# Optimization experiments

Measured on AMD Instinct MI355X. Metric: run time of the kernel, lower is better.

The kernel has to match this reference:

```python
import jax, jax.numpy as jnp
import numpy as np

N_NEURONS = 256
P_MAX = 8
N_BLOCKS = P_MAX + 1
HIDDEN = 32
BATCH = 8192


def setup_inputs() -> dict:
    key = jax.random.key(0)
    ks = jax.random.split(key, 9)
    z = jax.random.normal(ks[0], (BATCH, N_BLOCKS * N_NEURONS), dtype=jnp.float32)
    # Per-block ScalarMLP params, stacked over the n_blocks axis.
    s1 = 1.0 / np.sqrt(N_NEURONS)
    s2 = 1.0 / np.sqrt(HIDDEN)
    gW1 = jax.random.uniform(ks[1], (N_BLOCKS, N_NEURONS, HIDDEN), jnp.float32, -s1, s1)
    gb1 = jax.random.uniform(ks[2], (N_BLOCKS, HIDDEN), jnp.float32, -s1, s1)
    gW2 = jax.random.uniform(ks[3], (N_BLOCKS, HIDDEN, HIDDEN), jnp.float32, -s2, s2)
    gb2 = jax.random.uniform(ks[4], (N_BLOCKS, HIDDEN), jnp.float32, -s2, s2)
    gW3 = jax.random.uniform(ks[5], (N_BLOCKS, HIDDEN), jnp.float32, -s2, s2)
    gb3 = jax.random.uniform(ks[6], (N_BLOCKS,), jnp.float32, -s2, s2)
    # Lag coupling matrices W_r ~ U(-init_scale, init_scale), init_scale=0.1
    W = jax.random.uniform(ks[7], (P_MAX, N_NEURONS, N_NEURONS), jnp.float32, -0.1, 0.1)
    return {"z": z, "gW1": gW1, "gb1": gb1, "gW2": gW2, "gb2": gb2,
            "gW3": gW3, "gb3": gb3, "W": W}


def _energy(z, gW1, gb1, gW2, gb2, gW3, gb3, W):
    B = z.shape[0]
    blocks = z.reshape(B, N_BLOCKS, N_NEURONS)           # (B, K, n)
    # Per-block ScalarMLP energies (all blocks at once).
    h1 = jax.nn.silu(jnp.einsum('bkn,knh->bkh', blocks, gW1) + gb1)   # (B, K, H)
    h2 = jax.nn.silu(jnp.einsum('bkh,khg->bkg', h1, gW2) + gb2)       # (B, K, H)
    e = jnp.einsum('bkh,kh->bk', h2, gW3) + gb3                        # (B, K)
    # Bilinear lag couplings: z_future^T W_r z_{lag-r}, r = 1..p_max.
    z_future = blocks[:, P_MAX, :]                                     # (B, n)
    lags = blocks[:, :P_MAX, :][:, ::-1, :]                            # (B, p, n), index r-1 == block p_max-r
    cross = jnp.einsum('bi,rij,brj->b', z_future, W, lags)             # (B,)
    return e.sum(axis=-1) + cross                                      # (B,)


def reference(z, gW1, gb1, gW2, gb2, gW3, gb3, W):
    # Score s(z) = -grad_z U(z); sum over batch gives per-sample grads
    # since energies are independent across samples.
    grad_z = jax.grad(lambda zz: _energy(zz, gW1, gb1, gW2, gb2, gW3, gb3, W).sum())(z)
    return -grad_z
```

## Files before the change

### kernel.cpp

```cpp
#include <hip/hip_runtime.h>
#include <hip/hip_bf16.h>
#include <math.h>

#define BATCH 8192
#define NB 9
#define NN 256
#define PMAX 8
#define HID 32
#define ZDIM 2304

typedef short bf16x8 __attribute__((ext_vector_type(8)));
typedef float f32x4 __attribute__((ext_vector_type(4)));

static __device__ inline unsigned short f2bf(float f) {
    __hip_bfloat16 h = __float2bfloat16(f);
    return *reinterpret_cast<unsigned short*>(&h);
}

static __device__ inline uint4 pack8(float4 a, float4 b) {
    uint4 u;
    u.x = (unsigned)f2bf(a.x) | ((unsigned)f2bf(a.y) << 16);
    u.y = (unsigned)f2bf(a.z) | ((unsigned)f2bf(a.w) << 16);
    u.z = (unsigned)f2bf(b.x) | ((unsigned)f2bf(b.y) << 16);
    u.w = (unsigned)f2bf(b.z) | ((unsigned)f2bf(b.w) << 16);
    return u;
}

__global__ __launch_bounds__(256) void k_pack(
    const float* __restrict__ W, const float* __restrict__ gW1,
    unsigned short* __restrict__ Wb, unsigned short* __restrict__ WTb,
    unsigned short* __restrict__ gW1b, unsigned short* __restrict__ g1Tb) {
    int r = blockIdx.z;
    int t = threadIdx.x;
    if (r < 8) {
        __shared__ float tt[32][33];
        int i0 = blockIdx.y * 32;
        int j0 = blockIdx.x * 32;
        int tx = t & 31;
        int ty = t >> 5;
        const float* src = W + (size_t)r * 65536;
        #pragma unroll
        for (int s = 0; s < 32; s += 8) {
            float v = src[(size_t)(i0 + ty + s) * 256 + (j0 + tx)];
            tt[ty + s][tx] = v;
            Wb[(size_t)r * 65536 + (size_t)(i0 + ty + s) * 256 + (j0 + tx)] = f2bf(v);
        }
        __syncthreads();
        #pragma unroll
        for (int s = 0; s < 32; s += 8)
            WTb[(size_t)r * 65536 + (size_t)(j0 + ty + s) * 256 + (i0 + tx)] = f2bf(tt[tx][ty + s]);
    } else {
        int tg = (blockIdx.y * 8 + blockIdx.x) * 256 + t;
        for (int e = tg; e < 73728; e += 16384) {
            float v = gW1[e];
            unsigned short b = f2bf(v);
            gW1b[e] = b;
            int k = e >> 13, n = (e >> 5) & 255, h = e & 31;
            g1Tb[(size_t)(k * 32 + h) * 256 + n] = b;
        }
    }
}

__global__ __launch_bounds__(256) void k_mlp(
    const float* __restrict__ z, const unsigned short* __restrict__ g1Tb,
    const float* __restrict__ gb1, const float* __restrict__ gW2,
    const float* __restrict__ gb2, const float* __restrict__ gW3,
    float* __restrict__ d1ws) {
    __shared__ uint4 As4[2][512];
    __shared__ uint4 Bw[1024];
    __shared__ uint4 W2Ts4[128];
    __shared__ uint4 W2Ns4[128];

    int t = threadIdx.x;
    int lane = t & 63;
    int w = t >> 6;
    int k = blockIdx.y;
    int b0 = blockIdx.x * 128;

    const unsigned short* bsrc = g1Tb + (size_t)k * 8192;
    for (int e = t; e < 1024; e += 256) {
        int h = e >> 5;
        int rest = e & 31;
        int c = rest >> 2, qq = rest & 3;
        Bw[c * 128 + (h & 15) + 16 * qq + 64 * (h >> 4)] =
            *(const uint4*)(bsrc + (size_t)h * 256 + c * 32 + qq * 8);
    }
    const float* gw2 = gW2 + (size_t)k * 1024;
    unsigned short* w2t = (unsigned short*)W2Ts4;
    unsigned short* w2n = (unsigned short*)W2Ns4;
    for (int e = t; e < 1024; e += 256) {
        int n = e >> 5, kk = e & 31;
        int qq = kk >> 3, jj = kk & 7;
        int ci = (n & 15) + 16 * qq + 64 * (n >> 4);
        w2t[ci * 8 + jj] = f2bf(gw2[kk * 32 + n]);
        w2n[ci * 8 + jj] = f2bf(gw2[n * 32 + kk]);
    }

    int mq = t >> 2;
    int q = t & 3;
    int ci0 = (mq & 15) + 16 * q + 64 * (mq >> 4);

    f32x4 acc1[2][2];
    #pragma unroll
    for (int i = 0; i < 2; ++i)
        #pragma unroll
        for (int j = 0; j < 2; ++j) acc1[i][j] = (f32x4){0.f, 0.f, 0.f, 0.f};

    auto loadZ = [&](int c, float4 (&fa)[2][2]) {
        #pragma unroll
        for (int pp = 0; pp < 2; ++pp) {
            int m = mq + 64 * pp;
            const float* as = z + (size_t)(b0 + m) * ZDIM + k * 256 + c * 32 + q * 8;
            fa[pp][0] = *(const float4*)(as);
            fa[pp][1] = *(const float4*)(as + 4);
        }
    };
    auto storeA = [&](int buf, float4 (&fa)[2][2]) {
        #pragma unroll
        for (int pp = 0; pp < 2; ++pp)
            As4[buf][ci0 + 256 * pp] = pack8(fa[pp][0], fa[pp][1]);
    };

    {
        float4 fa[2][2];
        loadZ(0, fa);
        storeA(0, fa);
    }
    int cur = 0;
    for (int c = 0; c < 8; ++c) {
        __syncthreads();
        float4 fan[2][2];
        if (c < 7) loadZ(c + 1, fan);
        bf16x8 af[2], bfr[2];
        #pragma unroll
        for (int i = 0; i < 2; ++i) af[i] = __builtin_bit_cast(bf16x8, As4[cur][lane + (w * 2 + i) * 64]);
        #pragma unroll
        for (int j = 0; j < 2; ++j) bfr[j] = __builtin_bit_cast(bf16x8, Bw[c * 128 + lane + j * 64]);
        #pragma unroll
        for (int i = 0; i < 2; ++i)
            #pragma unroll
            for (int j = 0; j < 2; ++j)
                acc1[i][j] = __builtin_amdgcn_mfma_f32_16x16x32_bf16(af[i], bfr[j], acc1[i][j], 0, 0, 0);
        if (c < 7) storeA(cur ^ 1, fan);
        cur ^= 1;
    }

    int cq = lane >> 4;
    int ci16 = lane & 15;
    float b1v[2], b2v[2], g3v[2];
    #pragma unroll
    for (int j = 0; j < 2; ++j) {
        b1v[j] = gb1[k * 32 + j * 16 + ci16];
        b2v[j] = gb2[k * 32 + j * 16 + ci16];
        g3v[j] = gW3[k * 32 + j * 16 + ci16];
    }
    unsigned short* Hs = (unsigned short*)As4;
    float sp1[2][2][4];
    __syncthreads();
    #pragma unroll
    for (int i = 0; i < 2; ++i)
        #pragma unroll
        for (int j = 0; j < 2; ++j)
            #pragma unroll
            for (int r = 0; r < 4; ++r) {
                float a1 = acc1[i][j][r] + b1v[j];
                float s1 = 1.f / (1.f + __expf(-a1));
                sp1[i][j][r] = s1 * (1.f + a1 * (1.f - s1));
                int row = w * 32 + i * 16 + cq * 4 + r;
                int col = j * 16 + ci16;
                int chunk = (row & 15) + 16 * (col >> 3) + 64 * (row >> 4);
                Hs[chunk * 8 + (col & 7)] = f2bf(a1 * s1);
            }
    __syncthreads();

    bf16x8 af2[2], wf[2];
    #pragma unroll
    for (int i = 0; i < 2; ++i) af2[i] = __builtin_bit_cast(bf16x8, As4[0][lane + (w * 2 + i) * 64]);
    #pragma unroll
    for (int j = 0; j < 2; ++j) wf[j] = __builtin_bit_cast(bf16x8, W2Ts4[lane + j * 64]);
    f32x4 acc2[2][2];
    #pragma unroll
    for (int i = 0; i < 2; ++i)
        #pragma unroll
        for (int j = 0; j < 2; ++j) {
            acc2[i][j] = (f32x4){0.f, 0.f, 0.f, 0.f};
            acc2[i][j] = __builtin_amdgcn_mfma_f32_16x16x32_bf16(af2[i], wf[j], acc2[i][j], 0, 0, 0);
        }

    __syncthreads();
    #pragma unroll
    for (int i = 0; i < 2; ++i)
        #pragma unroll
        for (int j = 0; j < 2; ++j)
            #pragma unroll
            for (int r = 0; r < 4; ++r) {
                float a2 = acc2[i][j][r] + b2v[j];
                float s2 = 1.f / (1.f + __expf(-a2));
                float da2 = g3v[j] * s2 * (1.f + a2 * (1.f - s2));
                int row = w * 32 + i * 16 + cq * 4 + r;
                int col = j * 16 + ci16;
                int chunk = (row & 15) + 16 * (col >> 3) + 64 * (row >> 4);
                Hs[chunk * 8 + (col & 7)] = f2bf(da2);
            }
    __syncthreads();

    bf16x8 af3[2], wg[2];
    #pragma unroll
    for (int i = 0; i < 2; ++i) af3[i] = __builtin_bit_cast(bf16x8, As4[0][lane + (w * 2 + i) * 64]);
    #pragma unroll
    for (int j = 0; j < 2; ++j) wg[j] = __builtin_bit_cast(bf16x8, W2Ns4[lane + j * 64]);
    #pragma unroll
    for (int i = 0; i < 2; ++i)
        #pragma unroll
        for (int j = 0; j < 2; ++j) {
            f32x4 a3 = (f32x4){0.f, 0.f, 0.f, 0.f};
            a3 = __builtin_amdgcn_mfma_f32_16x16x32_bf16(af3[i], wg[j], a3, 0, 0, 0);
            #pragma unroll
            for (int r = 0; r < 4; ++r) {
                int row = w * 32 + i * 16 + cq * 4 + r;
                int col = j * 16 + ci16;
                d1ws[((size_t)k * BATCH + b0 + row) * 32 + col] = a3[r] * sp1[i][j][r];
            }
        }
}

__global__ __launch_bounds__(256) void k_gemm_lo(
    const float* __restrict__ z, const float* __restrict__ d1,
    const unsigned short* __restrict__ WTb, const unsigned short* __restrict__ gW1b,
    float* __restrict__ out) {
    __shared__ uint4 As4[2][512];
    __shared__ uint4 Bs4[2][512];

    int t = threadIdx.x;
    int lane = t & 63;
    int w = t >> 6;
    int wr = w >> 1, wc = w & 1;
    int b0 = blockIdx.x * 128;
    int n0 = blockIdx.y * 128;
    int k  = n0 >> 8;
    int jb = n0 & 255;

    const float* Amain = z + (size_t)b0 * ZDIM + 2048;
    const float* Aext  = d1 + ((size_t)k * BATCH + b0) * 32;
    const unsigned short* Bmain = WTb + (size_t)(7 - k) * 65536 + (size_t)jb * 256;
    const unsigned short* Bext  = gW1b + ((size_t)k * 256 + jb) * 32;

    int mq = t >> 2;
    int q  = t & 3;
    int ci0 = (mq & 15) + 16 * q + 64 * (mq >> 4);

    auto loadAB = [&](int c, float4 (&fa)[2][2], uint4 (&bu)[2]) {
        #pragma unroll
        for (int pp = 0; pp < 2; ++pp) {
            int m = mq + 64 * pp;
            const float* as = (c < 8) ? (Amain + (size_t)m * ZDIM + c * 32 + q * 8)
                                      : (Aext + (size_t)m * 32 + q * 8);
            fa[pp][0] = *(const float4*)(as);
            fa[pp][1] = *(const float4*)(as + 4);
            const unsigned short* bs = (c < 8) ? (Bmain + (size_t)m * 256 + c * 32 + q * 8)
                                               : (Bext + (size_t)m * 32 + q * 8);
            bu[pp] = *(const uint4*)(bs);
        }
    };
    auto storeAB = [&](int buf, float4 (&fa)[2][2], uint4 (&bu)[2]) {
        #pragma unroll
        for (int pp = 0; pp < 2; ++pp) {
            int idx = ci0 + 256 * pp;
            As4[buf][idx] = pack8(fa[pp][0], fa[pp][1]);
            Bs4[buf][idx] = bu[pp];
        }
    };

    f32x4 acc[4][4];
    #pragma unroll
    for (int i = 0; i < 4; ++i)
        #pragma unroll
        for (int j = 0; j < 4; ++j) acc[i][j] = (f32x4){0.f, 0.f, 0.f, 0.f};

    {
        float4 fa[2][2]; uint4 bu[2];
        loadAB(0, fa, bu);
        storeAB(0, fa, bu);
    }
    int cur = 0;
    for (int c = 0; c < 9; ++c) {
        __syncthreads();
        float4 fan[2][2]; uint4 bun[2];
        if (c < 8) loadAB(c + 1, fan, bun);
        bf16x8 af[4], bf[4];
        #pragma unroll
        for (int i = 0; i < 4; ++i) af[i] = __builtin_bit_cast(bf16x8, As4[cur][lane + (wr * 4 + i) * 64]);
        #pragma unroll
        for (int j = 0; j < 4; ++j) bf[j] = __builtin_bit_cast(bf16x8, Bs4[cur][lane + (wc * 4 + j) * 64]);
        #pragma unroll
        for (int i = 0; i < 4; ++i)
            #pragma unroll
            for (int j = 0; j < 4; ++j)
                acc[i][j] = __builtin_amdgcn_mfma_f32_16x16x32_bf16(af[i], bf[j], acc[i][j], 0, 0, 0);
        if (c < 8) storeAB(cur ^ 1, fan, bun);
        cur ^= 1;
    }

    int rquad = lane >> 4;
    int cidx  = lane & 15;
    #pragma unroll
    for (int i = 0; i < 4; ++i) {
        #pragma unroll
        for (int j = 0; j < 4; ++j) {
            float* o = out + (size_t)(b0 + wr * 64 + i * 16 + rquad * 4) * ZDIM
                     + (k * 256 + jb + wc * 64 + j * 16 + cidx);
            #pragma unroll
            for (int r = 0; r < 4; ++r)
                o[(size_t)r * ZDIM] = -acc[i][j][r];
        }
    }
}

__global__ __launch_bounds__(256) void k_gemm_hi(
    const float* __restrict__ z, const float* __restrict__ d1,
    const unsigned short* __restrict__ Wb, const unsigned short* __restrict__ gW1b,
    float* __restrict__ out) {
    __shared__ uint4 As4[2][512];
    __shared__ uint4 Bs4[2][512];

    int t = threadIdx.x;
    int lane = t & 63;
    int w = t >> 6;
    int wr = w & 1, wc = w >> 1;
    int b0 = blockIdx.x * 64;
    int i0 = blockIdx.y * 64;

    const float* Amain = z + (size_t)b0 * ZDIM;
    const float* Aext  = d1 + ((size_t)8 * BATCH + b0) * 32;
    const unsigned short* Bext = gW1b + (size_t)(8 * 256 + i0) * 32;

    int m = t >> 2;
    int q = t & 3;
    int ci = (m & 15) + 16 * q + 64 * (m >> 4);

    auto loadAB = [&](int c, float4 (&fa)[2][2], uint4 (&bu)[2]) {
        if (c < 32) {
            int kb = c * 64;
            #pragma unroll
            for (int h = 0; h < 2; ++h) {
                const float* as = Amain + (size_t)m * ZDIM + kb + h * 32 + q * 8;
                fa[h][0] = *(const float4*)(as);
                fa[h][1] = *(const float4*)(as + 4);
            }
            int lag = kb >> 8;
            int j0  = kb & 255;
            const unsigned short* bs = Wb + (size_t)(7 - lag) * 65536
                                         + (size_t)(i0 + m) * 256 + j0 + q * 8;
            bu[0] = *(const uint4*)(bs);
            bu[1] = *(const uint4*)(bs + 32);
        } else {
            const float* as = Aext + (size_t)m * 32 + q * 8;
            fa[0][0] = *(const float4*)(as);
            fa[0][1] = *(const float4*)(as + 4);
            fa[1][0] = make_float4(0.f, 0.f, 0.f, 0.f);
            fa[1][1] = make_float4(0.f, 0.f, 0.f, 0.f);
            bu[0] = *(const uint4*)(Bext + (size_t)m * 32 + q * 8);
            bu[1] = make_uint4(0u, 0u, 0u, 0u);
        }
    };
    auto storeAB = [&](int buf, float4 (&fa)[2][2], uint4 (&bu)[2]) {
        #pragma unroll
        for (int h = 0; h < 2; ++h) {
            As4[buf][h * 256 + ci] = pack8(fa[h][0], fa[h][1]);
            Bs4[buf][h * 256 + ci] = bu[h];
        }
    };

    f32x4 acc[2][2];
    #pragma unroll
    for (int i = 0; i < 2; ++i)
        #pragma unroll
        for (int j = 0; j < 2; ++j) acc[i][j] = (f32x4){0.f, 0.f, 0.f, 0.f};

    {
        float4 fa[2][2]; uint4 bu[2];
        loadAB(0, fa, bu);
        storeAB(0, fa, bu);
    }
    int cur = 0;
    for (int c = 0; c < 33; ++c) {
        __syncthreads();
        float4 fan[2][2]; uint4 bun[2];
        if (c < 32) loadAB(c + 1, fan, bun);
        #pragma unroll
        for (int h = 0; h < 2; ++h) {
            bf16x8 af[2], bf[2];
            #pragma unroll
            for (int i = 0; i < 2; ++i)
                af[i] = __builtin_bit_cast(bf16x8, As4[cur][h * 256 + lane + (wr * 2 + i) * 64]);
            #pragma unroll
            for (int j = 0; j < 2; ++j)
                bf[j] = __builtin_bit_cast(bf16x8, Bs4[cur][h * 256 + lane + (wc * 2 + j) * 64]);
            #pragma unroll
            for (int i = 0; i < 2; ++i)
                #pragma unroll
                for (int j = 0; j < 2; ++j)
                    acc[i][j] = __builtin_amdgcn_mfma_f32_16x16x32_bf16(af[i], bf[j], acc[i][j], 0, 0, 0);
        }
        if (c < 32) storeAB(cur ^ 1, fan, bun);
        cur ^= 1;
    }

    int rquad = lane >> 4;
    int cidx  = lane & 15;
    #pragma unroll
    for (int i = 0; i < 2; ++i) {
        #pragma unroll
        for (int j = 0; j < 2; ++j) {
            float* o = out + (size_t)(b0 + wr * 32 + i * 16 + rquad * 4) * ZDIM
                     + (2048 + i0 + wc * 32 + j * 16 + cidx);
            #pragma unroll
            for (int r = 0; r < 4; ++r)
                o[(size_t)r * ZDIM] = -acc[i][j][r];
        }
    }
}

extern "C" void kernel_launch(void* const* d_in, const int* in_sizes, int n_in,
                              void* d_out, int out_size, void* d_ws, size_t ws_size,
                              hipStream_t stream) {
    const float* z   = (const float*)d_in[0];
    const float* gW1 = (const float*)d_in[1];
    const float* gb1 = (const float*)d_in[2];
    const float* gW2 = (const float*)d_in[3];
    const float* gb2 = (const float*)d_in[4];
    const float* gW3 = (const float*)d_in[5];
    const float* W   = (const float*)d_in[7];
    float* out = (float*)d_out;

    float* ws = (float*)d_ws;
    float*          d1ws = ws;
    unsigned short* Wb   = (unsigned short*)(ws + 2359296);
    unsigned short* WTb  = Wb + 524288;
    unsigned short* gW1b = WTb + 524288;
    unsigned short* g1Tb = gW1b + 73728;

    k_pack<<<dim3(8, 8, 9), 256, 0, stream>>>(W, gW1, Wb, WTb, gW1b, g1Tb);
    k_mlp<<<dim3(64, 9), 256, 0, stream>>>(z, g1Tb, gb1, gW2, gb2, gW3, d1ws);
    k_gemm_lo<<<dim3(64, 16), 256, 0, stream>>>(z, d1ws, WTb, gW1b, out);
    k_gemm_hi<<<dim3(128, 4), 256, 0, stream>>>(z, d1ws, Wb, gW1b, out);
}
```

Before: 199.8 us.

## Drop LDS staging in k_gemm_hi; load MFMA fragments directly from global

The k_gemm_hi kernel no longer stages A and B tiles through double-buffered shared memory with block-wide barriers. Each wave now owns a 16-row strip and loads its bf16 A fragment (converted from fp32) and four B fragments straight from global memory into registers, with a one-step register prefetch. This removes LDS traffic and __syncthreads, but the four waves now each load B separately instead of sharing it, and global loads are narrower, so more global and L2 traffic results.

Result: slower. 260.1 us (+30.1%).

```diff
diff --git a/kernel.cpp b/kernel.cpp
--- a/kernel.cpp
+++ b/kernel.cpp
@@ -320,104 +320,71 @@
     const float* __restrict__ z, const float* __restrict__ d1,
     const unsigned short* __restrict__ Wb, const unsigned short* __restrict__ gW1b,
     float* __restrict__ out) {
-    __shared__ uint4 As4[2][512];
-    __shared__ uint4 Bs4[2][512];
-
     int t = threadIdx.x;
     int lane = t & 63;
     int w = t >> 6;
-    int wr = w & 1, wc = w >> 1;
     int b0 = blockIdx.x * 64;
     int i0 = blockIdx.y * 64;
 
-    const float* Amain = z + (size_t)b0 * ZDIM;
-    const float* Aext  = d1 + ((size_t)8 * BATCH + b0) * 32;
-    const unsigned short* Bext = gW1b + (size_t)(8 * 256 + i0) * 32;
-
-    int m = t >> 2;
-    int q = t & 3;
-    int ci = (m & 15) + 16 * q + 64 * (m >> 4);
-
-    auto loadAB = [&](int c, float4 (&fa)[2][2], uint4 (&bu)[2]) {
-        if (c < 32) {
-            int kb = c * 64;
-            #pragma unroll
-            for (int h = 0; h < 2; ++h) {
-                const float* as = Amain + (size_t)m * ZDIM + kb + h * 32 + q * 8;
-                fa[h][0] = *(const float4*)(as);
-                fa[h][1] = *(const float4*)(as + 4);
-            }
-            int lag = kb >> 8;
-            int j0  = kb & 255;
-            const unsigned short* bs = Wb + (size_t)(7 - lag) * 65536
-                                         + (size_t)(i0 + m) * 256 + j0 + q * 8;
-            bu[0] = *(const uint4*)(bs);
-            bu[1] = *(const uint4*)(bs + 32);
+    int rl = lane & 15;
+    int kq = lane >> 4;
+
+    const float* arow = z + (size_t)(b0 + w * 16 + rl) * ZDIM + kq * 8;
+    const float* atail = d1 + ((size_t)8 * BATCH + b0 + w * 16 + rl) * 32 + kq * 8;
+
+    f32x4 acc[4];
+    #pragma unroll
+    for (int j = 0; j < 4; ++j) acc[j] = (f32x4){0.f, 0.f, 0.f, 0.f};
+
+    auto loadA = [&](int c, float4& x0, float4& x1) {
+        const float* p = (c < 64) ? (arow + c * 32) : atail;
+        x0 = *(const float4*)(p);
+        x1 = *(const float4*)(p + 4);
+    };
+    auto loadB = [&](int c, uint4 (&bb)[4]) {
+        if (c < 64) {
+            int lag = c >> 3;
+            int j0  = (c & 7) * 32;
+            const unsigned short* base = Wb + (size_t)(7 - lag) * 65536 + j0 + kq * 8;
+            #pragma unroll
+            for (int j = 0; j < 4; ++j)
+                bb[j] = *(const uint4*)(base + (size_t)(i0 + j * 16 + rl) * 256);
         } else {
-            const float* as = Aext + (size_t)m * 32 + q * 8;
-            fa[0][0] = *(const float4*)(as);
-            fa[0][1] = *(const float4*)(as + 4);
-            fa[1][0] = make_float4(0.f, 0.f, 0.f, 0.f);
-            fa[1][1] = make_float4(0.f, 0.f, 0.f, 0.f);
-            bu[0] = *(const uint4*)(Bext + (size_t)m * 32 + q * 8);
-            bu[1] = make_uint4(0u, 0u, 0u, 0u);
-        }
-    };
-    auto storeAB = [&](int buf, float4 (&fa)[2][2], uint4 (&bu)[2]) {
-        #pragma unroll
-        for (int h = 0; h < 2; ++h) {
-            As4[buf][h * 256 + ci] = pack8(fa[h][0], fa[h][1]);
-            Bs4[buf][h * 256 + ci] = bu[h];
-        }
-    };
-
-    f32x4 acc[2][2];
-    #pragma unroll
-    for (int i = 0; i < 2; ++i)
-        #pragma unroll
-        for (int j = 0; j < 2; ++j) acc[i][j] = (f32x4){0.f, 0.f, 0.f, 0.f};
-
-    {
-        float4 fa[2][2]; uint4 bu[2];
-        loadAB(0, fa, bu);
-        storeAB(0, fa, bu);
-    }
-    int cur = 0;
-    for (int c = 0; c < 33; ++c) {
-        __syncthreads();
-        float4 fan[2][2]; uint4 bun[2];
-        if (c < 32) loadAB(c + 1, fan, bun);
-        #pragma unroll
-        for (int h = 0; h < 2; ++h) {
-            bf16x8 af[2], bf[2];
-            #pragma unroll
-            for (int i = 0; i < 2; ++i)
-                af[i] = __builtin_bit_cast(bf16x8, As4[cur][h * 256 + lane + (wr * 2 + i) * 64]);
-            #pragma unroll
-            for (int j = 0; j < 2; ++j)
-                bf[j] = __builtin_bit_cast(bf16x8, Bs4[cur][h * 256 + lane + (wc * 2 + j) * 64]);
-            #pragma unroll
-            for (int i = 0; i < 2; ++i)
-                #pragma unroll
-                for (int j = 0; j < 2; ++j)
-                    acc[i][j] = __builtin_amdgcn_mfma_f32_16x16x32_bf16(af[i], bf[j], acc[i][j], 0, 0, 0);
-        }
-        if (c < 32) storeAB(cur ^ 1, fan, bun);
-        cur ^= 1;
-    }
-
-    int rquad = lane >> 4;
-    int cidx  = lane & 15;
-    #pragma unroll
-    for (int i = 0; i < 2; ++i) {
-        #pragma unroll
-        for (int j = 0; j < 2; ++j) {
-            float* o = out + (size_t)(b0 + wr * 32 + i * 16 + rquad * 4) * ZDIM
-                     + (2048 + i0 + wc * 32 + j * 16 + cidx);
-            #pragma unroll
-            for (int r = 0; r < 4; ++r)
-                o[(size_t)r * ZDIM] = -acc[i][j][r];
-        }
+            #pragma unroll
+            for (int j = 0; j < 4; ++j)
+                bb[j] = *(const uint4*)(gW1b + (size_t)(8 * 256 + i0 + j * 16 + rl) * 32 + kq * 8);
+        }
+    };
+
+    float4 a0, a1;
+    uint4 bb[4];
+    loadA(0, a0, a1);
+    loadB(0, bb);
+    for (int c = 0; c < 65; ++c) {
+        float4 na0, na1;
+        uint4 nbb[4];
+        if (c < 64) {
+            loadA(c + 1, na0, na1);
+            loadB(c + 1, nbb);
+        }
+        bf16x8 af = __builtin_bit_cast(bf16x8, pack8(a0, a1));
+        #pragma unroll
+        for (int j = 0; j < 4; ++j)
+            acc[j] = __builtin_amdgcn_mfma_f32_16x16x32_bf16(
+                af, __builtin_bit_cast(bf16x8, bb[j]), acc[j], 0, 0, 0);
+        if (c < 64) {
+            a0 = na0; a1 = na1;
+            #pragma unroll
+            for (int j = 0; j < 4; ++j) bb[j] = nbb[j];
+        }
+    }
+
+    #pragma unroll
+    for (int j = 0; j < 4; ++j) {
+        float* o = out + (size_t)(b0 + w * 16 + kq * 4) * ZDIM + 2048 + i0 + j * 16 + rl;
+        #pragma unroll
+        for (int r = 0; r < 4; ++r)
+            o[(size_t)r * ZDIM] = -acc[j][r];
     }
 }
 
```
